# Kernel tuning notes

Measured on AMD Instinct MI355X. Metric: run time of the kernel, lower is better.

## Reference

```python
import jax, jax.numpy as jnp
import numpy as np

B, C, H, W = 4, 2048, 32, 32


def conv1x1(x, Wt, b):
    # 1x1 conv == per-pixel matmul over channels
    return jnp.einsum('oc,bchw->bohw', Wt, x) + b[None, :, None, None]


def cross_attention(Q, K, V):
    b, c, h, w = Q.shape
    q = Q.reshape(b, c, h * w)   # [B, C, N]
    k = K.reshape(b, c, h * w)
    v = V.reshape(b, c, h * w)
    scores = jnp.einsum('bcn,bcm->bnm', q, k) / jnp.sqrt(jnp.asarray(c, jnp.float32))
    attn = jax.nn.softmax(scores, axis=-1)          # [B, N, N]
    out = jnp.einsum('bcm,bnm->bcn', v, attn)       # V @ attn^T
    return out.reshape(b, c, h, w)


def setup_inputs() -> dict:
    key = jax.random.key(0)
    ks = jax.random.split(key, 14)
    d = {
        'F_rgb': jax.random.normal(ks[0], (B, C, H, W), jnp.float32),
        'F_indices': jax.random.normal(ks[1], (B, C, H, W), jnp.float32),
    }
    names = ['q_rgb', 'k_rgb', 'v_rgb', 'q_ind', 'k_ind', 'v_ind']
    for i, n in enumerate(names):
        d['W_' + n] = jax.random.normal(ks[2 + 2 * i], (C, C), jnp.float32) * 0.02
        d['b_' + n] = jax.random.normal(ks[3 + 2 * i], (C,), jnp.float32) * 0.01
    return d


def reference(F_rgb, F_indices, W_q_rgb, b_q_rgb, W_k_rgb, b_k_rgb, W_v_rgb, b_v_rgb,
              W_q_ind, b_q_ind, W_k_ind, b_k_ind, W_v_ind, b_v_ind):
    # RGB queries attend over index features
    Q_rgb = conv1x1(F_rgb, W_q_rgb, b_q_rgb)
    K_ind = conv1x1(F_indices, W_k_ind, b_k_ind)
    V_ind = conv1x1(F_indices, W_v_ind, b_v_ind)
    F_rgb_attended = cross_attention(Q_rgb, K_ind, V_ind)
    # Index queries attend over RGB features
    Q_ind = conv1x1(F_indices, W_q_ind, b_q_ind)
    K_rgb = conv1x1(F_rgb, W_k_rgb, b_k_rgb)
    V_rgb = conv1x1(F_rgb, W_v_rgb, b_v_rgb)
    F_ind_attended = cross_attention(Q_ind, K_rgb, V_rgb)
    F_final = F_rgb_attended + F_ind_attended
    attention_weights = jnp.stack([F_rgb_attended, F_ind_attended], axis=1)  # [B,2,C,H,W]
    # pre_attention_outputs is an identity passthrough of the inputs
    return (F_final, F_rgb, F_indices, attention_weights)
```

## Files before the change

kernel.cpp:

```cpp
#include <hip/hip_runtime.h>

typedef __bf16 bf16x8 __attribute__((ext_vector_type(8)));
typedef float  f32x4  __attribute__((ext_vector_type(4)));
typedef unsigned short u16;

__device__ __forceinline__ u16 f2bf(float f) {
  unsigned u = __builtin_bit_cast(unsigned, f);
  u += 0x7fffu + ((u >> 16) & 1u);
  return (u16)(u >> 16);
}

using gvoid = __attribute__((address_space(1))) void;
using svoid = __attribute__((address_space(3))) void;
__device__ __forceinline__ void load_lds16(const void* g, void* s) {
  __builtin_amdgcn_global_load_lds((const gvoid*)g, (svoid*)s, 16, 0, 0);
}

__global__ void transpose_cvt(const float* __restrict__ Fr, const float* __restrict__ Fi,
                              u16* __restrict__ FTr, u16* __restrict__ FTi,
                              float* __restrict__ Or, float* __restrict__ Oi) {
  __shared__ float tile[32][33];
  const int b = blockIdx.z & 3;
  const bool ind = (blockIdx.z >= 4);
  const float* F = ind ? Fi : Fr;
  u16* FT = ind ? FTi : FTr;
  float* O = ind ? Oi : Or;
  const int n0 = blockIdx.x * 32, c0 = blockIdx.y * 32;
  const long boff = (long)b * 2048 * 1024;
  const float* Fb = F + boff;
  float* Ob = O + boff;
  u16* FTb = FT + (long)b * 1024 * 2048;
  const int tx = threadIdx.x, ty = threadIdx.y;
#pragma unroll
  for (int i = 0; i < 4; ++i) {
    const long idx = (long)(c0 + ty + i * 8) * 1024 + n0 + tx;
    float v = Fb[idx];
    tile[ty + i * 8][tx] = v;
    Ob[idx] = v;
  }
  __syncthreads();
#pragma unroll
  for (int i = 0; i < 4; ++i)
    FTb[(long)(n0 + ty + i * 8) * 2048 + c0 + tx] = f2bf(tile[tx][ty + i * 8]);
}

__global__ void cvt6(const float* __restrict__ s0, const float* __restrict__ s1,
                     const float* __restrict__ s2, const float* __restrict__ s3,
                     const float* __restrict__ s4, const float* __restrict__ s5,
                     u16* __restrict__ dst) {
  const int blk = blockIdx.x;
  const int chunk = blk >> 12;
  const int i = (blk & 4095) * 256 + threadIdx.x;
  const float* src;
  switch (chunk) {
    case 0: src = s0; break; case 1: src = s1; break; case 2: src = s2; break;
    case 3: src = s3; break; case 4: src = s4; break; default: src = s5; break;
  }
  float4 v = ((const float4*)src)[i];
  ushort4 o;
  o.x = f2bf(v.x); o.y = f2bf(v.y); o.z = f2bf(v.z); o.w = f2bf(v.w);
  ((ushort4*)(dst + (long)chunk * 4194304))[i] = o;
}


#define BAR_ do { asm volatile("" ::: "memory"); __builtin_amdgcn_s_barrier(); \
                  asm volatile("" ::: "memory"); } while (0)
#define SB0 __builtin_amdgcn_sched_barrier(0)
#define LGK0 asm volatile("s_waitcnt lgkmcnt(0)" ::: "memory")
#define VMW6 asm volatile("s_waitcnt vmcnt(6)" ::: "memory")

#define b0A0 0
#define b0A1 16384
#define b0B0 32768
#define b0B1 49152
#define b1A0 65536
#define b1A1 81920
#define b1B0 98304
#define b1B1 114688

#define STG(Mp, ld, row0, kt, off)                                                 \
  do {                                                                             \
    load_lds16(Mp + (long)((row0) + w * 8 + srow) * (ld) + (kt) * 64 + scol,       \
               sm + (off) + w * 1024);                                             \
    load_lds16(Mp + (long)((row0) + 64 + w * 8 + srow) * (ld) + (kt) * 64 + scol,  \
               sm + (off) + 8192 + w * 1024);                                      \
  } while (0)

#define RDA(off)                                                                   \
  _Pragma("unroll") for (int fm = 0; fm < 4; ++fm)                                 \
  _Pragma("unroll") for (int ks = 0; ks < 2; ++ks)                                 \
    fa[fm][ks] = *(const bf16x8*)(sm + (off) + aoff[fm] + kin[ks]);

#define RDB(off, dst)                                                              \
  _Pragma("unroll") for (int fn = 0; fn < 2; ++fn)                                 \
  _Pragma("unroll") for (int ks = 0; ks < 2; ++ks)                                 \
    dst[fn][ks] = *(const bf16x8*)(sm + (off) + boff[fn] + kin[ks]);

#define MMQ(qa, qb, fb)                                                            \
  __builtin_amdgcn_s_setprio(1);                                                   \
  _Pragma("unroll") for (int ks = 0; ks < 2; ++ks)                                 \
  _Pragma("unroll") for (int fm = 0; fm < 4; ++fm)                                 \
  _Pragma("unroll") for (int fn = 0; fn < 2; ++fn)                                 \
    acc[qa][qb][fm][fn] = __builtin_amdgcn_mfma_f32_16x16x32_bf16(                 \
        fa[fm][ks], fb[fn][ks], acc[qa][qb][fm][fn], 0, 0, 0);                     \
  __builtin_amdgcn_s_setprio(0);

template <int OUT_BF16, int BIAS_MODE, int KSPLIT>
__global__ __launch_bounds__(512, 2) void gemm256(
    const u16* __restrict__ A0p, const u16* __restrict__ B0p, void* __restrict__ D0p,
    const float* __restrict__ ba0, const float* __restrict__ bb0,
    const u16* __restrict__ A1p, const u16* __restrict__ B1p, void* __restrict__ D1p,
    const float* __restrict__ ba1, const float* __restrict__ bb1,
    long sKH, int zsplit, int K, int lda, int ldb, int ldd,
    long sA, long sB, long sD) {
  __shared__ __attribute__((aligned(128))) char sm[131072];
  int zb = blockIdx.z;
  int kh = 0;
  if (KSPLIT) { kh = zb >> 3; zb &= 7; }
  const bool s1 = (zb >= zsplit);
  const int zz = s1 ? zb - zsplit : zb;
  const u16* Ag = (s1 ? A1p : A0p) + (long)zz * sA + (long)kh * K;
  const u16* Bg = (s1 ? B1p : B0p) + (long)zz * sB + (long)kh * K;
  char* Dg = (char*)(s1 ? D1p : D0p) + (long)zz * sD * (OUT_BF16 ? 2 : 4)
           + (KSPLIT ? (long)kh * sKH : 0L);
  const float* ba = s1 ? ba1 : ba0;
  const float* bb = s1 ? bb1 : bb0;
  const int m0 = blockIdx.y * 256, n0 = blockIdx.x * 256;
  const int t = threadIdx.x, w = t >> 6, l = t & 63;
  const int wr = w >> 2, wc = w & 3;
  const int lm = l & 15, lk = l >> 4;
  const int swz = (l & 7) << 4;
  const int srow = l >> 3;
  const int scol = ((l & 7) ^ srow) << 3;
  int aoff[4], boff[2], kin[2];
#pragma unroll
  for (int fm = 0; fm < 4; ++fm) aoff[fm] = (wr * 64 + fm * 16 + lm) * 128;
#pragma unroll
  for (int fn = 0; fn < 2; ++fn) boff[fn] = (wc * 32 + fn * 16 + lm) * 128;
  kin[0] = (lk * 16) ^ swz;
  kin[1] = (64 + lk * 16) ^ swz;

  f32x4 acc[2][2][4][2] = {};
  bf16x8 fa[4][2], fb0[2][2], fb1[2][2];

  const int nt = K >> 6;

  STG(Ag, lda, m0,       0, b0A0);
  STG(Bg, ldb, n0,       0, b0B0);
  STG(Bg, ldb, n0 + 128, 0, b0B1);
  STG(Ag, lda, m0 + 128, 0, b0A1);
  STG(Ag, lda, m0,       1, b1A0);
  STG(Bg, ldb, n0,       1, b1B0);
  STG(Bg, ldb, n0 + 128, 1, b1B1);
  VMW6;
  BAR_;
  RDB(b0B0, fb0);

  for (int v = 0; v < nt; v += 2) {
    const int t2 = (v + 2 < nt) ? v + 2 : nt - 1;
    const int t3 = (v + 3 < nt) ? v + 3 : nt - 1;
    STG(Ag, lda, m0 + 128, v + 1, b1A1);
    RDA(b0A0);
    BAR_; LGK0; SB0; MMQ(0, 0, fb0);
    RDB(b0B1, fb1);
    BAR_; LGK0; SB0; MMQ(0, 1, fb1);
    STG(Ag, lda, m0, t2, b0A0);
    STG(Bg, ldb, n0, t2, b0B0);
    RDA(b0A1);
    BAR_; LGK0; SB0; MMQ(1, 0, fb0);
    STG(Bg, ldb, n0 + 128, t2, b0B1);
    VMW6;
    BAR_; LGK0; SB0; MMQ(1, 1, fb1);
    RDB(b1B0, fb0);
    STG(Ag, lda, m0 + 128, t2, b0A1);
    RDA(b1A0);
    BAR_; LGK0; SB0; MMQ(0, 0, fb0);
    RDB(b1B1, fb1);
    BAR_; LGK0; SB0; MMQ(0, 1, fb1);
    STG(Ag, lda, m0, t3, b1A0);
    STG(Bg, ldb, n0, t3, b1B0);
    RDA(b1A1);
    BAR_; LGK0; SB0; MMQ(1, 0, fb0);
    STG(Bg, ldb, n0 + 128, t3, b1B1);
    VMW6;
    BAR_; LGK0; SB0; MMQ(1, 1, fb1);
    RDB(b0B0, fb0);
  }

#pragma unroll
  for (int qa = 0; qa < 2; ++qa)
#pragma unroll
    for (int qb = 0; qb < 2; ++qb)
#pragma unroll
      for (int fm = 0; fm < 4; ++fm)
#pragma unroll
        for (int fn = 0; fn < 2; ++fn) {
          const int row0 = m0 + qa * 128 + wr * 64 + fm * 16 + lk * 4;
          const int col  = n0 + qb * 128 + wc * 32 + fn * 16 + lm;
          float cb = 0.f;
          if (BIAS_MODE == 1) cb = (col < 2048) ? ba[col] : bb[col - 2048];
          f32x4 vv = acc[qa][qb][fm][fn];
#pragma unroll
          for (int j = 0; j < 4; ++j) {
            float x = vv[j] + cb;
            if (BIAS_MODE == 2) x += ba[row0 + j];
            const long idx = (long)(row0 + j) * ldd + col;
            if (OUT_BF16) ((u16*)Dg)[idx] = f2bf(x);
            else          ((float*)Dg)[idx] = x;
          }
        }
}

__global__ void softmax_rows2(const float* __restrict__ S0, const float* __restrict__ S1,
                              u16* __restrict__ P, float alpha) {
  const long row = blockIdx.x;
  const int t = threadIdx.x, l = t & 63, w = t >> 6;
  float4 a = ((const float4*)(S0 + row * 1024))[t];
  float4 b = ((const float4*)(S1 + row * 1024))[t];
  float4 v;
  v.x = a.x + b.x; v.y = a.y + b.y; v.z = a.z + b.z; v.w = a.w + b.w;
  __shared__ float red[8];
  float m = fmaxf(fmaxf(v.x, v.y), fmaxf(v.z, v.w));
#pragma unroll
  for (int off = 32; off; off >>= 1) m = fmaxf(m, __shfl_xor(m, off));
  if (l == 0) red[w] = m;
  __syncthreads();
  m = fmaxf(fmaxf(red[0], red[1]), fmaxf(red[2], red[3]));
  float e0 = __expf((v.x - m) * alpha);
  float e1 = __expf((v.y - m) * alpha);
  float e2 = __expf((v.z - m) * alpha);
  float e3 = __expf((v.w - m) * alpha);
  float s = e0 + e1 + e2 + e3;
#pragma unroll
  for (int off = 32; off; off >>= 1) s += __shfl_xor(s, off);
  if (l == 0) red[4 + w] = s;
  __syncthreads();
  s = red[4] + red[5] + red[6] + red[7];
  const float inv = 1.0f / s;
  ushort4 o;
  o.x = f2bf(e0 * inv); o.y = f2bf(e1 * inv);
  o.z = f2bf(e2 * inv); o.w = f2bf(e3 * inv);
  ((ushort4*)(P + row * 1024))[t] = o;
}

__global__ void final_add(const float4* __restrict__ aw, float4* __restrict__ dst) {
  const long i = (long)blockIdx.x * 256 + threadIdx.x;
  const long b = i >> 19;
  const long r = i & 524287;
  float4 a = aw[b * 1048576 + r];
  float4 c = aw[b * 1048576 + 524288 + r];
  float4 o;
  o.x = a.x + c.x; o.y = a.y + c.y; o.z = a.z + c.z; o.w = a.w + c.w;
  dst[i] = o;
}

extern "C" void kernel_launch(void* const* d_in, const int* in_sizes, int n_in,
                              void* d_out, int out_size, void* d_ws, size_t ws_size,
                              hipStream_t stream) {
  (void)in_sizes; (void)n_in; (void)out_size; (void)ws_size;
  const float* F_rgb = (const float*)d_in[0];
  const float* F_ind = (const float*)d_in[1];
  const float* bq_rgb = (const float*)d_in[3];
  const float* bk_rgb = (const float*)d_in[5];
  const float* bv_rgb = (const float*)d_in[7];
  const float* bq_ind = (const float*)d_in[9];
  const float* bk_ind = (const float*)d_in[11];
  const float* bv_ind = (const float*)d_in[13];

  char* ws = (char*)d_ws;
  u16* FT_rgb  = (u16*)(ws);
  u16* FT_ind  = (u16*)(ws + 16777216);
  float* S1    = (float*)(ws);
  u16* Wall    = (u16*)(ws + 33554432);
  u16* Wqk_rgb = Wall;
  u16* Wqk_ind = (u16*)(ws + 50331648);
  u16* Wv_rgb  = (u16*)(ws + 67108864);
  u16* Wv_ind  = (u16*)(ws + 75497472);
  u16* QKT_rgb = (u16*)(ws + 83886080);
  u16* QKT_ind = (u16*)(ws + 117440512);
  u16* V_rgb   = (u16*)(ws + 150994944);
  u16* V_ind   = (u16*)(ws + 167772160);
  float* S0    = (float*)(ws + 184549376);
  u16*   P     = (u16*)(ws + 218103808);

  float* out       = (float*)d_out;
  float* out_final = out;
  float* out_Frgb  = out + 8388608;
  float* out_Find  = out + 16777216;
  float* AW        = out + 25165824;

  transpose_cvt<<<dim3(32, 64, 8), dim3(32, 8), 0, stream>>>(
      F_rgb, F_ind, FT_rgb, FT_ind, out_Frgb, out_Find);
  cvt6<<<24576, 256, 0, stream>>>((const float*)d_in[2], (const float*)d_in[4],
                                  (const float*)d_in[8], (const float*)d_in[10],
                                  (const float*)d_in[6], (const float*)d_in[12], Wall);

  gemm256<1, 1, 0><<<dim3(16, 4, 8), 512, 0, stream>>>(
      FT_rgb, Wqk_rgb, QKT_rgb, bq_rgb, bk_rgb,
      FT_ind, Wqk_ind, QKT_ind, bq_ind, bk_ind,
      0L, 4, 2048, 2048, 2048, 4096, 2097152L, 0L, 4194304L);

  gemm256<1, 2, 0><<<dim3(4, 8, 8), 512, 0, stream>>>(
      Wv_rgb, FT_rgb, V_rgb, bv_rgb, bv_rgb,
      Wv_ind, FT_ind, V_ind, bv_ind, bv_ind,
      0L, 4, 2048, 2048, 2048, 1024, 0L, 2097152L, 2097152L);

  gemm256<0, 0, 1><<<dim3(4, 4, 16), 512, 0, stream>>>(
      QKT_rgb, QKT_ind + 2048, S0, nullptr, nullptr,
      QKT_ind, QKT_rgb + 2048, S0 + 4194304, nullptr, nullptr,
      (long)((char*)S1 - (char*)S0), 4, 1024, 4096, 4096, 1024,
      4194304L, 4194304L, 1048576L);

  softmax_rows2<<<8192, 256, 0, stream>>>(S0, S1, P, 0.02209708691207961f);

  gemm256<0, 0, 0><<<dim3(4, 8, 8), 512, 0, stream>>>(
      V_ind, P, AW, nullptr, nullptr,
      V_rgb, P + 4194304, AW + 2097152, nullptr, nullptr,
      0L, 4, 1024, 1024, 1024, 1024, 2097152L, 1048576L, 4194304L);

  final_add<<<8192, 256, 0, stream>>>((const float4*)AW, (float4*)out_final);
}
```

Before: 345.1 us.

## Merge MFMA quadrants, remap workgroups across XCDs, store split-K scores in bf16

The GEMM main loop now reads both B fragments up front and issues two quadrant MFMA groups per barrier instead of four, which halves the barrier count per k-step. Global loads are reordered to match the new schedule. Workgroup IDs are remapped so consecutive blocks spread across the XCDs. The split-K score partials are written as bf16 instead of fp32 and the softmax reads bf16, cutting score traffic at some cost in precision of the logits.

```diff
diff --git a/kernel.cpp b/kernel.cpp
--- a/kernel.cpp
+++ b/kernel.cpp
@@ -8,6 +8,9 @@
   unsigned u = __builtin_bit_cast(unsigned, f);
   u += 0x7fffu + ((u >> 16) & 1u);
   return (u16)(u >> 16);
+}
+__device__ __forceinline__ float bf2f(u16 h) {
+  return __builtin_bit_cast(float, (unsigned)h << 16);
 }
 
 using gvoid = __attribute__((address_space(1))) void;
@@ -96,13 +99,17 @@
   _Pragma("unroll") for (int ks = 0; ks < 2; ++ks)                                 \
     dst[fn][ks] = *(const bf16x8*)(sm + (off) + boff[fn] + kin[ks]);
 
-#define MMQ(qa, qb, fb)                                                            \
+#define MMQ2(qa)                                                                   \
   __builtin_amdgcn_s_setprio(1);                                                   \
   _Pragma("unroll") for (int ks = 0; ks < 2; ++ks)                                 \
-  _Pragma("unroll") for (int fm = 0; fm < 4; ++fm)                                 \
-  _Pragma("unroll") for (int fn = 0; fn < 2; ++fn)                                 \
-    acc[qa][qb][fm][fn] = __builtin_amdgcn_mfma_f32_16x16x32_bf16(                 \
-        fa[fm][ks], fb[fn][ks], acc[qa][qb][fm][fn], 0, 0, 0);                     \
+  _Pragma("unroll") for (int fm = 0; fm < 4; ++fm) {                               \
+    _Pragma("unroll") for (int fn = 0; fn < 2; ++fn)                               \
+      acc[qa][0][fm][fn] = __builtin_amdgcn_mfma_f32_16x16x32_bf16(                \
+          fa[fm][ks], fb0[fn][ks], acc[qa][0][fm][fn], 0, 0, 0);                   \
+    _Pragma("unroll") for (int fn = 0; fn < 2; ++fn)                               \
+      acc[qa][1][fm][fn] = __builtin_amdgcn_mfma_f32_16x16x32_bf16(                \
+          fa[fm][ks], fb1[fn][ks], acc[qa][1][fm][fn], 0, 0, 0);                   \
+  }                                                                                \
   __builtin_amdgcn_s_setprio(0);
 
 template <int OUT_BF16, int BIAS_MODE, int KSPLIT>
@@ -114,7 +121,14 @@
     long sKH, int zsplit, int K, int lda, int ldb, int ldd,
     long sA, long sB, long sD) {
   __shared__ __attribute__((aligned(128))) char sm[131072];
-  int zb = blockIdx.z;
+  const int gx = gridDim.x, gy = gridDim.y;
+  const int nwg = gx * gy * (int)gridDim.z;
+  const int lin = blockIdx.x + gx * (blockIdx.y + gy * blockIdx.z);
+  const int qch = nwg >> 3;
+  int swzid = (lin & 7) * qch + (lin >> 3);
+  const int bx = swzid % gx; swzid /= gx;
+  const int by = swzid % gy;
+  int zb = swzid / gy;
   int kh = 0;
   if (KSPLIT) { kh = zb >> 3; zb &= 7; }
   const bool s1 = (zb >= zsplit);
@@ -125,7 +139,7 @@
            + (KSPLIT ? (long)kh * sKH : 0L);
   const float* ba = s1 ? ba1 : ba0;
   const float* bb = s1 ? bb1 : bb0;
-  const int m0 = blockIdx.y * 256, n0 = blockIdx.x * 256;
+  const int m0 = by * 256, n0 = bx * 256;
   const int t = threadIdx.x, w = t >> 6, l = t & 63;
   const int wr = w >> 2, wc = w & 3;
   const int lm = l & 15, lk = l >> 4;
@@ -154,37 +168,28 @@
   STG(Bg, ldb, n0 + 128, 1, b1B1);
   VMW6;
   BAR_;
-  RDB(b0B0, fb0);
 
   for (int v = 0; v < nt; v += 2) {
     const int t2 = (v + 2 < nt) ? v + 2 : nt - 1;
     const int t3 = (v + 3 < nt) ? v + 3 : nt - 1;
     STG(Ag, lda, m0 + 128, v + 1, b1A1);
-    RDA(b0A0);
-    BAR_; LGK0; SB0; MMQ(0, 0, fb0);
-    RDB(b0B1, fb1);
-    BAR_; LGK0; SB0; MMQ(0, 1, fb1);
+    RDA(b0A0); RDB(b0B0, fb0); RDB(b0B1, fb1);
+    BAR_; LGK0; SB0; MMQ2(0);
     STG(Ag, lda, m0, t2, b0A0);
     STG(Bg, ldb, n0, t2, b0B0);
+    STG(Bg, ldb, n0 + 128, t2, b0B1);
     RDA(b0A1);
-    BAR_; LGK0; SB0; MMQ(1, 0, fb0);
-    STG(Bg, ldb, n0 + 128, t2, b0B1);
     VMW6;
-    BAR_; LGK0; SB0; MMQ(1, 1, fb1);
-    RDB(b1B0, fb0);
+    BAR_; LGK0; SB0; MMQ2(1);
     STG(Ag, lda, m0 + 128, t2, b0A1);
-    RDA(b1A0);
-    BAR_; LGK0; SB0; MMQ(0, 0, fb0);
-    RDB(b1B1, fb1);
-    BAR_; LGK0; SB0; MMQ(0, 1, fb1);
+    RDA(b1A0); RDB(b1B0, fb0); RDB(b1B1, fb1);
+    BAR_; LGK0; SB0; MMQ2(0);
     STG(Ag, lda, m0, t3, b1A0);
     STG(Bg, ldb, n0, t3, b1B0);
+    STG(Bg, ldb, n0 + 128, t3, b1B1);
     RDA(b1A1);
-    BAR_; LGK0; SB0; MMQ(1, 0, fb0);
-    STG(Bg, ldb, n0 + 128, t3, b1B1);
     VMW6;
-    BAR_; LGK0; SB0; MMQ(1, 1, fb1);
-    RDB(b0B0, fb0);
+    BAR_; LGK0; SB0; MMQ2(1);
   }
 
 #pragma unroll
@@ -211,25 +216,27 @@
         }
 }
 
-__global__ void softmax_rows2(const float* __restrict__ S0, const float* __restrict__ S1,
+__global__ void softmax_rows2(const u16* __restrict__ S0, const u16* __restrict__ S1,
                               u16* __restrict__ P, float alpha) {
   const long row = blockIdx.x;
   const int t = threadIdx.x, l = t & 63, w = t >> 6;
-  float4 a = ((const float4*)(S0 + row * 1024))[t];
-  float4 b = ((const float4*)(S1 + row * 1024))[t];
-  float4 v;
-  v.x = a.x + b.x; v.y = a.y + b.y; v.z = a.z + b.z; v.w = a.w + b.w;
+  ushort4 a = ((const ushort4*)(S0 + row * 1024))[t];
+  ushort4 b = ((const ushort4*)(S1 + row * 1024))[t];
+  float v0 = bf2f(a.x) + bf2f(b.x);
+  float v1 = bf2f(a.y) + bf2f(b.y);
+  float v2 = bf2f(a.z) + bf2f(b.z);
+  float v3 = bf2f(a.w) + bf2f(b.w);
   __shared__ float red[8];
-  float m = fmaxf(fmaxf(v.x, v.y), fmaxf(v.z, v.w));
+  float m = fmaxf(fmaxf(v0, v1), fmaxf(v2, v3));
 #pragma unroll
   for (int off = 32; off; off >>= 1) m = fmaxf(m, __shfl_xor(m, off));
   if (l == 0) red[w] = m;
   __syncthreads();
   m = fmaxf(fmaxf(red[0], red[1]), fmaxf(red[2], red[3]));
-  float e0 = __expf((v.x - m) * alpha);
-  float e1 = __expf((v.y - m) * alpha);
-  float e2 = __expf((v.z - m) * alpha);
-  float e3 = __expf((v.w - m) * alpha);
+  float e0 = __expf((v0 - m) * alpha);
+  float e1 = __expf((v1 - m) * alpha);
+  float e2 = __expf((v2 - m) * alpha);
+  float e3 = __expf((v3 - m) * alpha);
   float s = e0 + e1 + e2 + e3;
 #pragma unroll
   for (int off = 32; off; off >>= 1) s += __shfl_xor(s, off);
@@ -270,7 +277,7 @@
   char* ws = (char*)d_ws;
   u16* FT_rgb  = (u16*)(ws);
   u16* FT_ind  = (u16*)(ws + 16777216);
-  float* S1    = (float*)(ws);
+  u16* S1c     = (u16*)(ws);
   u16* Wall    = (u16*)(ws + 33554432);
   u16* Wqk_rgb = Wall;
   u16* Wqk_ind = (u16*)(ws + 50331648);
@@ -280,8 +287,8 @@
   u16* QKT_ind = (u16*)(ws + 117440512);
   u16* V_rgb   = (u16*)(ws + 150994944);
   u16* V_ind   = (u16*)(ws + 167772160);
-  float* S0    = (float*)(ws + 184549376);
-  u16*   P     = (u16*)(ws + 218103808);
+  u16* S0c     = (u16*)(ws + 184549376);
+  u16* P       = (u16*)(ws + 218103808);
 
   float* out       = (float*)d_out;
   float* out_final = out;
@@ -305,13 +312,13 @@
       Wv_ind, FT_ind, V_ind, bv_ind, bv_ind,
       0L, 4, 2048, 2048, 2048, 1024, 0L, 2097152L, 2097152L);
 
-  gemm256<0, 0, 1><<<dim3(4, 4, 16), 512, 0, stream>>>(
-      QKT_rgb, QKT_ind + 2048, S0, nullptr, nullptr,
-      QKT_ind, QKT_rgb + 2048, S0 + 4194304, nullptr, nullptr,
-      (long)((char*)S1 - (char*)S0), 4, 1024, 4096, 4096, 1024,
+  gemm256<1, 0, 1><<<dim3(4, 4, 16), 512, 0, stream>>>(
+      QKT_rgb, QKT_ind + 2048, S0c, nullptr, nullptr,
+      QKT_ind, QKT_rgb + 2048, S0c + 4194304, nullptr, nullptr,
+      (long)((char*)S1c - (char*)S0c), 4, 1024, 4096, 4096, 1024,
       4194304L, 4194304L, 1048576L);
 
-  softmax_rows2<<<8192, 256, 0, stream>>>(S0, S1, P, 0.02209708691207961f);
+  softmax_rows2<<<8192, 256, 0, stream>>>(S0c, S1c, P, 0.02209708691207961f);
 
   gemm256<0, 0, 0><<<dim3(4, 8, 8), 512, 0, stream>>>(
       V_ind, P, AW, nullptr, nullptr,
```

After: 329.4 us. 1.05x faster.
